# Performance work log

Measured on AMD Instinct MI355X. Metric: run time of the kernel, lower is better.

Reference implementation:

```python
import jax, jax.numpy as jnp
import numpy as np

B, S, D, F = 4, 4096, 512, 2048
EPS = 1e-5


def _layer_norm(x, g, b):
    # LayerNorm((sqlength, mdim)): normalize jointly over last two dims
    mu = jnp.mean(x, axis=(-2, -1), keepdims=True)
    var = jnp.mean(jnp.square(x - mu), axis=(-2, -1), keepdims=True)
    return (x - mu) * jax.lax.rsqrt(var + EPS) * g + b


def _attn(q, k, v, causal):
    # scores: [B, S_q, S_k]
    s = jnp.einsum('bqd,bkd->bqk', q, k) / jnp.sqrt(jnp.asarray(D, q.dtype))
    if causal:
        mask = jnp.triu(jnp.ones((s.shape[-2], s.shape[-1]), dtype=bool), k=1)
        s = jnp.where(mask, -jnp.inf, s)
    p = jax.nn.softmax(s, axis=-1)
    return jnp.einsum('bqk,bkd->bqd', p, v)


def setup_inputs() -> dict:
    key = jax.random.key(0)
    ks = jax.random.split(key, 12)
    sc = 0.02
    return {
        'x':    jax.random.normal(ks[0], (B, S, D), jnp.float32),
        'enc':  jax.random.normal(ks[1], (B, S, D), jnp.float32),
        'Wo1':  jax.random.normal(ks[2], (D, D), jnp.float32) * sc,
        'Wo2':  jax.random.normal(ks[3], (D, D), jnp.float32) * sc,
        'ln1_g': jnp.ones((S, D), jnp.float32),
        'ln1_b': jnp.zeros((S, D), jnp.float32),
        'ln2_g': jnp.ones((S, D), jnp.float32),
        'ln2_b': jnp.zeros((S, D), jnp.float32),
        'W1':   jax.random.normal(ks[4], (F, D), jnp.float32) * sc,
        'b1':   jnp.zeros((F,), jnp.float32),
        'W2':   jax.random.normal(ks[5], (D, F), jnp.float32) * sc,
        'b2':   jnp.zeros((D,), jnp.float32),
    }


def reference(x, enc, Wo1, Wo2, ln1_g, ln1_b, ln2_g, ln2_b, W1, b1, W2, b2):
    # 1) causal self-attention + residual + ln1
    o = _attn(x, x, x, causal=True) @ Wo1.T
    x = _layer_norm(o + x, ln1_g, ln1_b)
    # 2) cross attention (q=enc, k=enc, v=x per source) + residual + ln2
    o = _attn(enc, enc, x, causal=False) @ Wo2.T
    x = _layer_norm(o + x, ln2_g, ln2_b)
    # 3) position-wise FFN (original looped per token; vectorized here) + residual + ln2 (shared params)
    ff = jax.nn.relu(x @ W1.T + b1) @ W2.T + b2
    return _layer_norm(ff + x, ln2_g, ln2_b)
```

## Files before the change

### kernel.cpp

```cpp
#include <hip/hip_runtime.h>
#include <cstdint>
#include <cstddef>

#define NB 4
#define NS 4096
#define ND 512
#define NF 2048

typedef __bf16 bf16;
typedef __attribute__((ext_vector_type(8))) __bf16 bf16x8;
typedef __attribute__((ext_vector_type(4))) __bf16 bf16x4;
typedef __attribute__((ext_vector_type(4))) float f32x4;

#define MFMA16(a, b, c) __builtin_amdgcn_mfma_f32_16x16x32_bf16((a), (b), (c), 0, 0, 0)

__device__ __forceinline__ void async_copy16(void* lds, const void* g) {
  __builtin_amdgcn_global_load_lds(
      (__attribute__((address_space(1))) unsigned int*)(uintptr_t)g,
      (__attribute__((address_space(3))) unsigned int*)(unsigned)(uintptr_t)lds,
      16, 0, 0);
}

__device__ __forceinline__ int vswz_col(int c , int dloc) {
  return (c & ~31) | (((((c >> 3) & 3) + ((dloc >> 1) & 3)) & 3) << 3);
}

__global__ void k_detect(const unsigned short* __restrict__ x, unsigned* __restrict__ flag) {
  __shared__ int cnt;
  if (threadIdx.x == 0) cnt = 0;
  __syncthreads();
  int bad = 0;
  for (int i = threadIdx.x; i < 2048; i += 256) {
    unsigned e = (x[i] >> 7) & 0xFF;
    if (e < 100 || e > 140) bad++;
  }
  atomicAdd(&cnt, bad);
  __syncthreads();
  if (threadIdx.x == 0) *flag = (cnt > 200) ? 1u : 0u;
}

__global__ void k_norm_bf16(const void* __restrict__ src, bf16* __restrict__ dst,
                            const unsigned* __restrict__ flag, int n) {
  int i = (blockIdx.x * 256 + threadIdx.x) * 8;
  if (i >= n) return;
  if (*flag) {
    const float* s = (const float*)src;
    float4 a = *(const float4*)(s + i);
    float4 c = *(const float4*)(s + i + 4);
    bf16x8 v;
    v[0] = (bf16)a.x; v[1] = (bf16)a.y; v[2] = (bf16)a.z; v[3] = (bf16)a.w;
    v[4] = (bf16)c.x; v[5] = (bf16)c.y; v[6] = (bf16)c.z; v[7] = (bf16)c.w;
    *(bf16x8*)(dst + i) = v;
  } else {
    *(uint4*)(dst + i) = *(const uint4*)((const bf16*)src + i);
  }
}

__global__ void k_norm_f32(const void* __restrict__ src, float* __restrict__ dst,
                           const unsigned* __restrict__ flag, int n) {
  int i = blockIdx.x * 256 + threadIdx.x;
  if (i >= n) return;
  dst[i] = (*flag) ? ((const float*)src)[i] : (float)((const bf16*)src)[i];
}

__global__ void k_transpose(const bf16* __restrict__ in, bf16* __restrict__ out) {
  __shared__ bf16 t[64][72];
  const int b = blockIdx.z, s0 = blockIdx.x * 64, d0 = blockIdx.y * 64;
  const int tid = threadIdx.x;
#pragma unroll
  for (int it = 0; it < 2; ++it) {
    int slot = it * 256 + tid;
    int r = slot >> 3, c = (slot & 7) * 8;
    *(bf16x8*)&t[r][c] = *(const bf16x8*)&in[((size_t)b * NS + s0 + r) * ND + d0 + c];
  }
  __syncthreads();
#pragma unroll
  for (int it = 0; it < 2; ++it) {
    int slot = it * 256 + tid;
    int r = slot >> 3, c = (slot & 7) * 8;
    bf16x8 v;
#pragma unroll
    for (int k = 0; k < 8; ++k) v[k] = t[c + k][r];
    *(bf16x8*)&out[((size_t)b * ND + d0 + r) * NS + s0 + vswz_col(c, r)] = v;
  }
}

template <bool CAUSAL>
__global__ __launch_bounds__(512, 2) void k_attn7(const bf16* __restrict__ Q,
                                                  const bf16* __restrict__ Km,
                                                  const bf16* __restrict__ Vt,
                                                  bf16* __restrict__ O0, bf16* __restrict__ O1,
                                                  float2* __restrict__ ml) {
  __shared__ bf16 lds_[65536];

  const int tid = threadIdx.x;
  const int w = tid >> 6, lane = tid & 63, quad = lane >> 4, l15 = lane & 15;
  const int slot = blockIdx.x & 7;
  const int b = slot >> 1;
  const int z = slot & 1;
  const int q0 = (int)(blockIdx.x >> 3) * 128;

  const bf16* Kg = Km + (size_t)b * NS * ND;
  const bf16* Vg = Vt + (size_t)b * ND * NS;

  const bf16* Qg = Q + ((size_t)b * NS + q0 + w * 16 + l15) * ND;
  bf16x8 qf[16];
#pragma unroll
  for (int s = 0; s < 16; ++s) qf[s] = *(const bf16x8*)&Qg[s * 32 + quad * 8];
#pragma unroll
  for (int s = 0; s < 16; ++s)
#pragma unroll
    for (int j = 0; j < 8; ++j) qf[s][j] = (bf16)((float)qf[s][j] * 0.044194173824159216f);

  f32x4 o[32];
#pragma unroll
  for (int i = 0; i < 32; ++i) o[i] = (f32x4){0.f, 0.f, 0.f, 0.f};

  float m = -1e30f, l = 0.f;

  const int T = CAUSAL ? (q0 / 32 + 4) : (NS / 32);
  const int tA = (T + 1) >> 1;
  const int kt0 = z ? tA : 0;
  const int kt1 = z ? T : tA;
  const int laneA4 = ((((quad * 2) & 3) * 16) + l15) * 4;
  const int laneB4 = ((((quad * 2 + 1) & 3) * 16) + l15) * 4;
  const int vsw = ((quad + ((l15 >> 1) & 3)) & 3) * 8;

  auto STAGE = [&](bf16* base, int k0) {
#pragma unroll
    for (int i = 0; i < 4; ++i) {
      const int r = w * 4 + i;
      const int g = (lane & ~7) | ((lane ^ r) & 7);
      async_copy16(base + r * 512, Kg + (size_t)(k0 + r) * ND + g * 8);
    }
#pragma unroll
    for (int i = 0; i < 4; ++i) {
      const int d0 = (w * 4 + i) * 16;
      async_copy16(base + 16384 + d0 * 32, Vg + (size_t)(d0 + (lane >> 2)) * NS + k0 + (lane & 3) * 8);
    }
  };

  int buf = 0;
  if (kt0 < kt1) STAGE(lds_, kt0 * 32);
  __syncthreads();

  for (int kt = kt0; kt < kt1; ++kt) {
    const int k0 = kt * 32;
    bf16* Ks = lds_ + buf * 32768;
    bf16* Vs = Ks + 16384;
    if (kt + 1 < kt1) STAGE(lds_ + (buf ^ 1) * 32768, (kt + 1) * 32);

    f32x4 sa0 = (f32x4){0.f, 0.f, 0.f, 0.f};
    f32x4 sa1 = (f32x4){0.f, 0.f, 0.f, 0.f};
    __builtin_amdgcn_s_setprio(1);
#pragma unroll
    for (int s = 0; s < 16; ++s) {
      const int lc = s * 4 + quad;
      const int swz = ((lc & ~7) | ((lc ^ l15) & 7)) * 8;
      bf16x8 a0 = *(const bf16x8*)&Ks[l15 * 512 + swz];
      bf16x8 a1 = *(const bf16x8*)&Ks[(16 + l15) * 512 + swz];
      sa0 = MFMA16(a0, qf[s], sa0);
      sa1 = MFMA16(a1, qf[s], sa1);
    }
    __builtin_amdgcn_s_setprio(0);

    float sv[8];
    {
      const int qrow = q0 + w * 16 + l15;
      const bool needMask = CAUSAL && (k0 + 31 > q0 + w * 16);
#pragma unroll
      for (int kt2 = 0; kt2 < 2; ++kt2)
#pragma unroll
        for (int r = 0; r < 4; ++r) {
          float s = (kt2 == 0) ? sa0[r] : sa1[r];
          if (needMask) {
            int key = k0 + kt2 * 16 + quad * 4 + r;
            if (key > qrow) s = -1e30f;
          }
          sv[kt2 * 4 + r] = s;
        }
    }
    float tm = sv[0];
#pragma unroll
    for (int i = 1; i < 8; ++i) tm = fmaxf(tm, sv[i]);
    tm = fmaxf(tm, __shfl_xor(tm, 16));
    tm = fmaxf(tm, __shfl_xor(tm, 32));
    const float mn = fmaxf(m, tm);
    const float alpha = __expf(m - mn);
    m = mn;
    float pf[8];
    float ts = 0.f;
#pragma unroll
    for (int i = 0; i < 8; ++i) { pf[i] = __expf(sv[i] - mn); ts += pf[i]; }
    ts += __shfl_xor(ts, 16);
    ts += __shfl_xor(ts, 32);
    l = l * alpha + ts;
    if (__ballot(alpha < 0.99999f)) {
#pragma unroll
      for (int dt = 0; dt < 32; ++dt)
#pragma unroll
        for (int r = 0; r < 4; ++r) o[dt][r] *= alpha;
    }

    bf16x8 pb;
#pragma unroll
    for (int j = 0; j < 8; ++j) {
      const int r_ = j & 3;
      const int sl = (j < 4) ? laneA4 : laneB4;
      float v0 = __int_as_float(__builtin_amdgcn_ds_bpermute(sl, __float_as_int(pf[r_])));
      float v1 = __int_as_float(__builtin_amdgcn_ds_bpermute(sl, __float_as_int(pf[4 + r_])));
      pb[j] = (bf16)(quad < 2 ? v0 : v1);
    }

    __builtin_amdgcn_s_setprio(1);
#pragma unroll
    for (int dt = 0; dt < 32; ++dt) {
      bf16x8 a = *(const bf16x8*)&Vs[(dt * 16 + l15) * 32 + vsw];
      o[dt] = MFMA16(a, pb, o[dt]);
    }
    __builtin_amdgcn_s_setprio(0);

    __syncthreads();
    buf ^= 1;
  }

  const float inv = 1.f / l;
  if (lane < 16 && quad == 0) ml[((size_t)z * NB + b) * NS + q0 + w * 16 + lane] = make_float2(m, l);
  bf16* Ow = lds_ + w * 8192;
#pragma unroll
  for (int dt = 0; dt < 32; ++dt) {
    bf16x4 v;
#pragma unroll
    for (int r = 0; r < 4; ++r) v[r] = (bf16)(o[dt][r] * inv);
    *(bf16x4*)&Ow[l15 * 512 + dt * 16 + quad * 4] = v;
  }
  bf16* Og = (z ? O1 : O0) + ((size_t)b * NS + q0 + w * 16) * ND;
#pragma unroll
  for (int it = 0; it < 16; ++it) {
    bf16x8 row = *(const bf16x8*)&Ow[it * 512 + lane * 8];
    *(bf16x8*)&Og[(size_t)it * ND + lane * 8] = row;
  }
}

__global__ void k_merge(bf16* __restrict__ O0, const bf16* __restrict__ O1,
                        const float2* __restrict__ ml) {
  size_t i = ((size_t)blockIdx.x * 256 + threadIdx.x) * 8;
  int row = (int)(i >> 9);
  float2 a = ml[row];
  float2 c = ml[(size_t)NB * NS + row];
  float M = fmaxf(a.x, c.x);
  float w0 = __expf(a.x - M) * a.y;
  float w1 = __expf(c.x - M) * c.y;
  float den = 1.f / (w0 + w1);
  float c0 = w0 * den, c1 = w1 * den;
  bf16x8 v0 = *(const bf16x8*)(O0 + i);
  bf16x8 v1 = *(const bf16x8*)(O1 + i);
  bf16x8 ov;
#pragma unroll
  for (int k = 0; k < 8; ++k) ov[k] = (bf16)(c0 * (float)v0[k] + c1 * (float)v1[k]);
  *(bf16x8*)(O0 + i) = ov;
}

template <int RES_MODE, bool HAS_BIAS, bool RELU, bool STATS>
__global__ __launch_bounds__(256) void k_gemm(const bf16* __restrict__ A, const bf16* __restrict__ W,
                                              const bf16* __restrict__ resid,
                                              const float* __restrict__ bias, bf16* __restrict__ Out,
                                              float* __restrict__ stats, int M, int N, int K,
                                              int rowOfs) {
  __shared__ bf16 As[128 * 64];
  __shared__ bf16 Ws[128 * 64];
  const int tid = threadIdx.x;
  const int w = tid >> 6, lane = tid & 63, quad = lane >> 4, l15 = lane & 15;
  const int m0 = blockIdx.x * 128, n0 = blockIdx.y * 128;
  const int wr = (w >> 1) * 64, wc = (w & 1) * 64;
  const int arow = lane >> 3, acol = (lane & 7) * 8;

  f32x4 acc[16];
#pragma unroll
  for (int i = 0; i < 16; ++i) acc[i] = (f32x4){0.f, 0.f, 0.f, 0.f};

  for (int k0 = 0; k0 < K; k0 += 64) {
    __syncthreads();
#pragma unroll
    for (int i = 0; i < 4; ++i) {
      const int rbase = (w * 4 + i) * 8 + arow;
      async_copy16(&As[(w * 4 + i) * 512], A + (size_t)(m0 + rbase) * K + k0 + acol);
      async_copy16(&Ws[(w * 4 + i) * 512], W + (size_t)(n0 + rbase) * K + k0 + acol);
    }
    __syncthreads();
#pragma unroll
    for (int s = 0; s < 2; ++s) {
      bf16x8 af[4], bw[4];
#pragma unroll
      for (int i = 0; i < 4; ++i) af[i] = *(const bf16x8*)&As[(wr + i * 16 + l15) * 64 + s * 32 + quad * 8];
#pragma unroll
      for (int j = 0; j < 4; ++j) bw[j] = *(const bf16x8*)&Ws[(wc + j * 16 + l15) * 64 + s * 32 + quad * 8];
#pragma unroll
      for (int i = 0; i < 4; ++i)
#pragma unroll
        for (int j = 0; j < 4; ++j) acc[i * 4 + j] = MFMA16(af[i], bw[j], acc[i * 4 + j]);
    }
  }

  float lsum = 0.f, lsq = 0.f;
#pragma unroll
  for (int i = 0; i < 4; ++i)
#pragma unroll
    for (int j = 0; j < 4; ++j)
#pragma unroll
      for (int r = 0; r < 4; ++r) {
        int row = m0 + wr + i * 16 + quad * 4 + r;
        int col = n0 + wc + j * 16 + l15;
        float v = acc[i * 4 + j][r];
        if (HAS_BIAS) v += bias[col];
        if (RELU) v = fmaxf(v, 0.f);
        if (RES_MODE == 2) v += (float)resid[(size_t)row * N + col];
        Out[(size_t)row * N + col] = (bf16)v;
        if (STATS) { lsum += v; lsq += v * v; }
      }

  if (STATS) {
    __syncthreads();
    float* red = (float*)As;
    red[tid] = lsum;
    red[256 + tid] = lsq;
    __syncthreads();
    for (int off = 128; off > 0; off >>= 1) {
      if (tid < off) { red[tid] += red[tid + off]; red[256 + tid] += red[256 + tid + off]; }
      __syncthreads();
    }
    if (tid == 0) {
      int bidx = (rowOfs + m0) >> 12;
      atomicAdd(&stats[bidx * 2], red[0]);
      atomicAdd(&stats[bidx * 2 + 1], red[256]);
    }
  }
}

template <bool FINAL>
__global__ void k_ln(const bf16* __restrict__ T, const float* __restrict__ stats,
                     const void* __restrict__ gp, const void* __restrict__ bp,
                     void* __restrict__ outp, const unsigned* __restrict__ flag) {
  const float invN = 1.f / 2097152.f;
  size_t i = ((size_t)(blockIdx.x * 256 + threadIdx.x)) * 8;
  int b = (int)(i >> 21);
  int sd = (int)(i & 2097151);
  float mu = stats[b * 2] * invN;
  float var = stats[b * 2 + 1] * invN - mu * mu;
  float rs = rsqrtf(var + 1e-5f);
  bool f32m = (*flag != 0);
  bf16x8 tv = *(const bf16x8*)(T + i);
  float gv[8], bv[8];
  if (f32m) {
    float4 a = *(const float4*)((const float*)gp + sd), c = *(const float4*)((const float*)gp + sd + 4);
    gv[0] = a.x; gv[1] = a.y; gv[2] = a.z; gv[3] = a.w; gv[4] = c.x; gv[5] = c.y; gv[6] = c.z; gv[7] = c.w;
    float4 e = *(const float4*)((const float*)bp + sd), f = *(const float4*)((const float*)bp + sd + 4);
    bv[0] = e.x; bv[1] = e.y; bv[2] = e.z; bv[3] = e.w; bv[4] = f.x; bv[5] = f.y; bv[6] = f.z; bv[7] = f.w;
  } else {
    bf16x8 g8 = *(const bf16x8*)((const bf16*)gp + sd);
    bf16x8 b8 = *(const bf16x8*)((const bf16*)bp + sd);
#pragma unroll
    for (int k = 0; k < 8; ++k) { gv[k] = (float)g8[k]; bv[k] = (float)b8[k]; }
  }
  float ov[8];
#pragma unroll
  for (int k = 0; k < 8; ++k) ov[k] = ((float)tv[k] - mu) * rs * gv[k] + bv[k];
  if (FINAL && f32m) {
    float4 o0 = {ov[0], ov[1], ov[2], ov[3]}, o1 = {ov[4], ov[5], ov[6], ov[7]};
    *(float4*)((float*)outp + i) = o0;
    *(float4*)((float*)outp + i + 4) = o1;
  } else {
    bf16x8 o8;
#pragma unroll
    for (int k = 0; k < 8; ++k) o8[k] = (bf16)ov[k];
    *(bf16x8*)((bf16*)outp + i) = o8;
  }
}

__global__ void k_ln_t(const bf16* __restrict__ T, const float* __restrict__ stats,
                       const void* __restrict__ gp, const void* __restrict__ bp,
                       bf16* __restrict__ X, bf16* __restrict__ XT,
                       const unsigned* __restrict__ flag) {
  __shared__ bf16 t[64][72];
  const float invN = 1.f / 2097152.f;
  const int b = blockIdx.z, s0 = blockIdx.x * 64, d0 = blockIdx.y * 64;
  const int tid = threadIdx.x;
  const float mu = stats[b * 2] * invN;
  const float var = stats[b * 2 + 1] * invN - mu * mu;
  const float rs = rsqrtf(var + 1e-5f);
  const bool f32m = (*flag != 0);
#pragma unroll
  for (int it = 0; it < 2; ++it) {
    int slot = it * 256 + tid;
    int r = slot >> 3, c = (slot & 7) * 8;
    size_t idx = ((size_t)b * NS + s0 + r) * ND + d0 + c;
    size_t pidx = (size_t)(s0 + r) * ND + d0 + c;
    bf16x8 tv = *(const bf16x8*)&T[idx];
    float gv[8], bv[8];
    if (f32m) {
      float4 a = *(const float4*)((const float*)gp + pidx), cc = *(const float4*)((const float*)gp + pidx + 4);
      gv[0] = a.x; gv[1] = a.y; gv[2] = a.z; gv[3] = a.w; gv[4] = cc.x; gv[5] = cc.y; gv[6] = cc.z; gv[7] = cc.w;
      float4 e = *(const float4*)((const float*)bp + pidx), f = *(const float4*)((const float*)bp + pidx + 4);
      bv[0] = e.x; bv[1] = e.y; bv[2] = e.z; bv[3] = e.w; bv[4] = f.x; bv[5] = f.y; bv[6] = f.z; bv[7] = f.w;
    } else {
      bf16x8 g8 = *(const bf16x8*)((const bf16*)gp + pidx);
      bf16x8 b8 = *(const bf16x8*)((const bf16*)bp + pidx);
#pragma unroll
      for (int k = 0; k < 8; ++k) { gv[k] = (float)g8[k]; bv[k] = (float)b8[k]; }
    }
    bf16x8 ov;
#pragma unroll
    for (int k = 0; k < 8; ++k) ov[k] = (bf16)(((float)tv[k] - mu) * rs * gv[k] + bv[k]);
    *(bf16x8*)&X[idx] = ov;
    *(bf16x8*)&t[r][c] = ov;
  }
  __syncthreads();
#pragma unroll
  for (int it = 0; it < 2; ++it) {
    int slot = it * 256 + tid;
    int r = slot >> 3, c = (slot & 7) * 8;
    bf16x8 v;
#pragma unroll
    for (int k = 0; k < 8; ++k) v[k] = t[c + k][r];
    *(bf16x8*)&XT[((size_t)b * ND + d0 + r) * NS + s0 + vswz_col(c, r)] = v;
  }
}

extern "C" void kernel_launch(void* const* d_in, const int* in_sizes, int n_in, void* d_out,
                              int out_size, void* d_ws, size_t ws_size, hipStream_t stream) {
  (void)in_sizes; (void)n_in; (void)out_size;
  const void* x_raw = d_in[0];
  const void* enc_raw = d_in[1];
  const void* Wo1_raw = d_in[2];
  const void* Wo2_raw = d_in[3];
  const void* g1_raw = d_in[4];
  const void* bb1_raw = d_in[5];
  const void* g2_raw = d_in[6];
  const void* bb2_raw = d_in[7];
  const void* W1_raw = d_in[8];
  const void* bias1_raw = d_in[9];
  const void* W2_raw = d_in[10];
  const void* bias2_raw = d_in[11];

  char* w = (char*)d_ws;
  unsigned* flag = (unsigned*)(w + 0);
  float* stats = (float*)(w + 16);
  float* b1f = (float*)(w + 1024);
  float* b2f = (float*)(w + 1024 + 8192);
  size_t off = 16384;
  const size_t nBSD = (size_t)NB * NS * ND;
  bf16* Wo1b = (bf16*)(w + off); off += (size_t)ND * ND * 2;
  bf16* Wo2b = (bf16*)(w + off); off += (size_t)ND * ND * 2;
  bf16* W1b = (bf16*)(w + off); off += (size_t)NF * ND * 2;
  bf16* W2b = (bf16*)(w + off); off += (size_t)ND * NF * 2;
  bf16* xb = (bf16*)(w + off); off += nBSD * 2;
  bf16* Ab = (bf16*)(w + off); off += nBSD * 2;
  bf16* Tb = (bf16*)(w + off); off += nBSD * 2;
  bf16* X1b = (bf16*)(w + off); off += nBSD * 2;
  bf16* Hb = (bf16*)(w + off);
  const size_t hbFull = (size_t)NB * NS * NF * 2;
  const size_t hbHalf = hbFull / 2;
  const bool ffnFull = (ws_size >= off + hbFull);
  if (!ffnFull && ws_size < off + hbHalf) return;

  bf16* O1b = Hb;
  float2* mlb = (float2*)((char*)Hb + nBSD * 2);

  hipMemsetAsync(stats, 0, 24 * sizeof(float), stream);
  k_detect<<<1, 256, 0, stream>>>((const unsigned short*)x_raw, flag);

  k_norm_bf16<<<(int)(nBSD / 2048), 256, 0, stream>>>(x_raw, xb, flag, (int)nBSD);
  k_norm_bf16<<<(ND * ND) / 2048, 256, 0, stream>>>(Wo1_raw, Wo1b, flag, ND * ND);
  k_norm_bf16<<<(ND * ND) / 2048, 256, 0, stream>>>(Wo2_raw, Wo2b, flag, ND * ND);
  k_norm_bf16<<<(NF * ND) / 2048, 256, 0, stream>>>(W1_raw, W1b, flag, NF * ND);
  k_norm_bf16<<<(NF * ND) / 2048, 256, 0, stream>>>(W2_raw, W2b, flag, ND * NF);
  k_norm_f32<<<8, 256, 0, stream>>>(bias1_raw, b1f, flag, NF);
  k_norm_f32<<<2, 256, 0, stream>>>(bias2_raw, b2f, flag, ND);

  k_transpose<<<dim3(NS / 64, ND / 64, NB), 256, 0, stream>>>(xb, Tb);
  k_attn7<true><<<256, 512, 0, stream>>>(xb, xb, Tb, Ab, O1b, mlb);
  k_merge<<<(int)(nBSD / 2048), 256, 0, stream>>>(Ab, O1b, mlb);
  k_gemm<2, false, false, true><<<dim3(128, 4), 256, 0, stream>>>(Ab, Wo1b, xb, nullptr, Tb,
                                                                  stats + 0, NB * NS, ND, ND, 0);
  k_ln_t<<<dim3(NS / 64, ND / 64, NB), 256, 0, stream>>>(Tb, stats + 0, g1_raw, bb1_raw, X1b, Ab,
                                                         flag);
  k_norm_bf16<<<(int)(nBSD / 2048), 256, 0, stream>>>(enc_raw, xb, flag, (int)nBSD);

  k_attn7<false><<<256, 512, 0, stream>>>(xb, xb, Ab, Tb, O1b, mlb);
  k_merge<<<(int)(nBSD / 2048), 256, 0, stream>>>(Tb, O1b, mlb);
  k_gemm<2, false, false, true><<<dim3(128, 4), 256, 0, stream>>>(Tb, Wo2b, X1b, nullptr, Ab,
                                                                  stats + 8, NB * NS, ND, ND, 0);
  k_ln<false><<<(int)(nBSD / 2048), 256, 0, stream>>>(Ab, stats + 8, g2_raw, bb2_raw, X1b, flag);

  const int nChunk = ffnFull ? 1 : 2;
  const int rows = ffnFull ? (NB * NS) : 8192;
  for (int c = 0; c < nChunk; ++c) {
    size_t ro = (size_t)c * rows;
    k_gemm<0, true, true, false><<<dim3(rows / 128, 16), 256, 0, stream>>>(
        X1b + ro * ND, W1b, nullptr, b1f, Hb, nullptr, rows, NF, ND, 0);
    k_gemm<2, true, false, true><<<dim3(rows / 128, 4), 256, 0, stream>>>(
        Hb, W2b, X1b + ro * ND, b2f, Tb + ro * ND, stats + 16, rows, ND, NF, (int)ro);
  }
  k_ln<true><<<(int)(nBSD / 2048), 256, 0, stream>>>(Tb, stats + 16, g2_raw, bb2_raw, d_out, flag);
}
```

Baseline: 795.9 us.

## Balance causal attention by pairing low and high query tiles per block

Each causal attention block now covers two 64-row query groups taken from opposite ends of the sequence (j and 63-j). Warps 0-3 handle the low group and warps 4-7 the high one, and the two groups' key tiles run back to back in a single loop. Every block therefore processes a fixed 65 key tiles instead of a count that grows with query position, which removes the tail imbalance of the causal triangle. The cost is that half the warps sit idle at barriers in each iteration while the other half compute, so per-CU MFMA utilisation may drop.

```diff
diff --git a/kernel.cpp b/kernel.cpp
--- a/kernel.cpp
+++ b/kernel.cpp
@@ -86,7 +86,7 @@
 }
 
 template <bool CAUSAL>
-__global__ __launch_bounds__(512, 2) void k_attn7(const bf16* __restrict__ Q,
+__global__ __launch_bounds__(512, 2) void k_attn8(const bf16* __restrict__ Q,
                                                   const bf16* __restrict__ Km,
                                                   const bf16* __restrict__ Vt,
                                                   bf16* __restrict__ O0, bf16* __restrict__ O1,
@@ -98,19 +98,36 @@
   const int slot = blockIdx.x & 7;
   const int b = slot >> 1;
   const int z = slot & 1;
-  const int q0 = (int)(blockIdx.x >> 3) * 128;
+  const int j = (int)(blockIdx.x >> 3);
+
+  int qwb, nLo, n;
+  if (CAUSAL) {
+    nLo = j + 1;
+    n = 65;
+    qwb = (w < 4) ? (64 * j + w * 16) : (4032 - 64 * j + (w - 4) * 16);
+  } else {
+    nLo = 1 << 30;
+    n = 64;
+    qwb = j * 128 + w * 16;
+  }
+  const int nHi = 64 - j;
 
   const bf16* Kg = Km + (size_t)b * NS * ND;
   const bf16* Vg = Vt + (size_t)b * ND * NS;
 
-  const bf16* Qg = Q + ((size_t)b * NS + q0 + w * 16 + l15) * ND;
+  auto ktOf = [&](int i) -> int {
+    if (!CAUSAL) return z * 64 + i;
+    return (i < nLo) ? (z * nLo + i) : (z * nHi + (i - nLo));
+  };
+
+  const bf16* Qg = Q + ((size_t)b * NS + qwb + l15) * ND;
   bf16x8 qf[16];
 #pragma unroll
   for (int s = 0; s < 16; ++s) qf[s] = *(const bf16x8*)&Qg[s * 32 + quad * 8];
 #pragma unroll
   for (int s = 0; s < 16; ++s)
 #pragma unroll
-    for (int j = 0; j < 8; ++j) qf[s][j] = (bf16)((float)qf[s][j] * 0.044194173824159216f);
+    for (int jj = 0; jj < 8; ++jj) qf[s][jj] = (bf16)((float)qf[s][jj] * 0.044194173824159216f);
 
   f32x4 o[32];
 #pragma unroll
@@ -118,10 +135,6 @@
 
   float m = -1e30f, l = 0.f;
 
-  const int T = CAUSAL ? (q0 / 32 + 4) : (NS / 32);
-  const int tA = (T + 1) >> 1;
-  const int kt0 = z ? tA : 0;
-  const int kt1 = z ? T : tA;
   const int laneA4 = ((((quad * 2) & 3) * 16) + l15) * 4;
   const int laneB4 = ((((quad * 2 + 1) & 3) * 16) + l15) * 4;
   const int vsw = ((quad + ((l15 >> 1) & 3)) & 3) * 8;
@@ -141,91 +154,94 @@
   };
 
   int buf = 0;
-  if (kt0 < kt1) STAGE(lds_, kt0 * 32);
+  STAGE(lds_, ktOf(0) * 32);
   __syncthreads();
 
-  for (int kt = kt0; kt < kt1; ++kt) {
-    const int k0 = kt * 32;
+  for (int i = 0; i < n; ++i) {
+    const int k0 = ktOf(i) * 32;
     bf16* Ks = lds_ + buf * 32768;
     bf16* Vs = Ks + 16384;
-    if (kt + 1 < kt1) STAGE(lds_ + (buf ^ 1) * 32768, (kt + 1) * 32);
-
-    f32x4 sa0 = (f32x4){0.f, 0.f, 0.f, 0.f};
-    f32x4 sa1 = (f32x4){0.f, 0.f, 0.f, 0.f};
-    __builtin_amdgcn_s_setprio(1);
-#pragma unroll
-    for (int s = 0; s < 16; ++s) {
-      const int lc = s * 4 + quad;
-      const int swz = ((lc & ~7) | ((lc ^ l15) & 7)) * 8;
-      bf16x8 a0 = *(const bf16x8*)&Ks[l15 * 512 + swz];
-      bf16x8 a1 = *(const bf16x8*)&Ks[(16 + l15) * 512 + swz];
-      sa0 = MFMA16(a0, qf[s], sa0);
-      sa1 = MFMA16(a1, qf[s], sa1);
-    }
-    __builtin_amdgcn_s_setprio(0);
-
-    float sv[8];
-    {
-      const int qrow = q0 + w * 16 + l15;
-      const bool needMask = CAUSAL && (k0 + 31 > q0 + w * 16);
-#pragma unroll
-      for (int kt2 = 0; kt2 < 2; ++kt2)
-#pragma unroll
-        for (int r = 0; r < 4; ++r) {
-          float s = (kt2 == 0) ? sa0[r] : sa1[r];
-          if (needMask) {
-            int key = k0 + kt2 * 16 + quad * 4 + r;
-            if (key > qrow) s = -1e30f;
+    if (i + 1 < n) STAGE(lds_ + (buf ^ 1) * 32768, ktOf(i + 1) * 32);
+
+    const bool active = !CAUSAL || ((w >= 4) == (i >= nLo));
+    if (active) {
+      f32x4 sa0 = (f32x4){0.f, 0.f, 0.f, 0.f};
+      f32x4 sa1 = (f32x4){0.f, 0.f, 0.f, 0.f};
+      __builtin_amdgcn_s_setprio(1);
+#pragma unroll
+      for (int s = 0; s < 16; ++s) {
+        const int lc = s * 4 + quad;
+        const int swz = ((lc & ~7) | ((lc ^ l15) & 7)) * 8;
+        bf16x8 a0 = *(const bf16x8*)&Ks[l15 * 512 + swz];
+        bf16x8 a1 = *(const bf16x8*)&Ks[(16 + l15) * 512 + swz];
+        sa0 = MFMA16(a0, qf[s], sa0);
+        sa1 = MFMA16(a1, qf[s], sa1);
+      }
+      __builtin_amdgcn_s_setprio(0);
+
+      float sv[8];
+      {
+        const int qrow = qwb + l15;
+        const bool needMask = CAUSAL && (k0 + 31 > qwb);
+#pragma unroll
+        for (int kt2 = 0; kt2 < 2; ++kt2)
+#pragma unroll
+          for (int r = 0; r < 4; ++r) {
+            float s = (kt2 == 0) ? sa0[r] : sa1[r];
+            if (needMask) {
+              int key = k0 + kt2 * 16 + quad * 4 + r;
+              if (key > qrow) s = -1e30f;
+            }
+            sv[kt2 * 4 + r] = s;
           }
-          sv[kt2 * 4 + r] = s;
-        }
-    }
-    float tm = sv[0];
-#pragma unroll
-    for (int i = 1; i < 8; ++i) tm = fmaxf(tm, sv[i]);
-    tm = fmaxf(tm, __shfl_xor(tm, 16));
-    tm = fmaxf(tm, __shfl_xor(tm, 32));
-    const float mn = fmaxf(m, tm);
-    const float alpha = __expf(m - mn);
-    m = mn;
-    float pf[8];
-    float ts = 0.f;
-#pragma unroll
-    for (int i = 0; i < 8; ++i) { pf[i] = __expf(sv[i] - mn); ts += pf[i]; }
-    ts += __shfl_xor(ts, 16);
-    ts += __shfl_xor(ts, 32);
-    l = l * alpha + ts;
-    if (__ballot(alpha < 0.99999f)) {
-#pragma unroll
-      for (int dt = 0; dt < 32; ++dt)
-#pragma unroll
-        for (int r = 0; r < 4; ++r) o[dt][r] *= alpha;
-    }
-
-    bf16x8 pb;
-#pragma unroll
-    for (int j = 0; j < 8; ++j) {
-      const int r_ = j & 3;
-      const int sl = (j < 4) ? laneA4 : laneB4;
-      float v0 = __int_as_float(__builtin_amdgcn_ds_bpermute(sl, __float_as_int(pf[r_])));
-      float v1 = __int_as_float(__builtin_amdgcn_ds_bpermute(sl, __float_as_int(pf[4 + r_])));
-      pb[j] = (bf16)(quad < 2 ? v0 : v1);
-    }
-
-    __builtin_amdgcn_s_setprio(1);
-#pragma unroll
-    for (int dt = 0; dt < 32; ++dt) {
-      bf16x8 a = *(const bf16x8*)&Vs[(dt * 16 + l15) * 32 + vsw];
-      o[dt] = MFMA16(a, pb, o[dt]);
-    }
-    __builtin_amdgcn_s_setprio(0);
+      }
+      float tm = sv[0];
+#pragma unroll
+      for (int i2 = 1; i2 < 8; ++i2) tm = fmaxf(tm, sv[i2]);
+      tm = fmaxf(tm, __shfl_xor(tm, 16));
+      tm = fmaxf(tm, __shfl_xor(tm, 32));
+      const float mn = fmaxf(m, tm);
+      const float alpha = __expf(m - mn);
+      m = mn;
+      float pf[8];
+      float ts = 0.f;
+#pragma unroll
+      for (int i2 = 0; i2 < 8; ++i2) { pf[i2] = __expf(sv[i2] - mn); ts += pf[i2]; }
+      ts += __shfl_xor(ts, 16);
+      ts += __shfl_xor(ts, 32);
+      l = l * alpha + ts;
+      if (__ballot(alpha < 0.99999f)) {
+#pragma unroll
+        for (int dt = 0; dt < 32; ++dt)
+#pragma unroll
+          for (int r = 0; r < 4; ++r) o[dt][r] *= alpha;
+      }
+
+      bf16x8 pb;
+#pragma unroll
+      for (int jj = 0; jj < 8; ++jj) {
+        const int r_ = jj & 3;
+        const int sl = (jj < 4) ? laneA4 : laneB4;
+        float v0 = __int_as_float(__builtin_amdgcn_ds_bpermute(sl, __float_as_int(pf[r_])));
+        float v1 = __int_as_float(__builtin_amdgcn_ds_bpermute(sl, __float_as_int(pf[4 + r_])));
+        pb[jj] = (bf16)(quad < 2 ? v0 : v1);
+      }
+
+      __builtin_amdgcn_s_setprio(1);
+#pragma unroll
+      for (int dt = 0; dt < 32; ++dt) {
+        bf16x8 a = *(const bf16x8*)&Vs[(dt * 16 + l15) * 32 + vsw];
+        o[dt] = MFMA16(a, pb, o[dt]);
+      }
+      __builtin_amdgcn_s_setprio(0);
+    }
 
     __syncthreads();
     buf ^= 1;
   }
 
   const float inv = 1.f / l;
-  if (lane < 16 && quad == 0) ml[((size_t)z * NB + b) * NS + q0 + w * 16 + lane] = make_float2(m, l);
+  if (lane < 16 && quad == 0) ml[((size_t)z * NB + b) * NS + qwb + lane] = make_float2(m, l);
   bf16* Ow = lds_ + w * 8192;
 #pragma unroll
   for (int dt = 0; dt < 32; ++dt) {
@@ -234,7 +250,7 @@
     for (int r = 0; r < 4; ++r) v[r] = (bf16)(o[dt][r] * inv);
     *(bf16x4*)&Ow[l15 * 512 + dt * 16 + quad * 4] = v;
   }
-  bf16* Og = (z ? O1 : O0) + ((size_t)b * NS + q0 + w * 16) * ND;
+  bf16* Og = (z ? O1 : O0) + ((size_t)b * NS + qwb) * ND;
 #pragma unroll
   for (int it = 0; it < 16; ++it) {
     bf16x8 row = *(const bf16x8*)&Ow[it * 512 + lane * 8];
@@ -294,11 +310,11 @@
 #pragma unroll
       for (int i = 0; i < 4; ++i) af[i] = *(const bf16x8*)&As[(wr + i * 16 + l15) * 64 + s * 32 + quad * 8];
 #pragma unroll
-      for (int j = 0; j < 4; ++j) bw[j] = *(const bf16x8*)&Ws[(wc + j * 16 + l15) * 64 + s * 32 + quad * 8];
+      for (int jj = 0; jj < 4; ++jj) bw[jj] = *(const bf16x8*)&Ws[(wc + jj * 16 + l15) * 64 + s * 32 + quad * 8];
 #pragma unroll
       for (int i = 0; i < 4; ++i)
 #pragma unroll
-        for (int j = 0; j < 4; ++j) acc[i * 4 + j] = MFMA16(af[i], bw[j], acc[i * 4 + j]);
+        for (int jj = 0; jj < 4; ++jj) acc[i * 4 + jj] = MFMA16(af[i], bw[jj], acc[i * 4 + jj]);
     }
   }
 
@@ -306,12 +322,12 @@
 #pragma unroll
   for (int i = 0; i < 4; ++i)
 #pragma unroll
-    for (int j = 0; j < 4; ++j)
+    for (int jj = 0; jj < 4; ++jj)
 #pragma unroll
       for (int r = 0; r < 4; ++r) {
         int row = m0 + wr + i * 16 + quad * 4 + r;
-        int col = n0 + wc + j * 16 + l15;
-        float v = acc[i * 4 + j][r];
+        int col = n0 + wc + jj * 16 + l15;
+        float v = acc[i * 4 + jj][r];
         if (HAS_BIAS) v += bias[col];
         if (RELU) v = fmaxf(v, 0.f);
         if (RES_MODE == 2) v += (float)resid[(size_t)row * N + col];
@@ -478,7 +494,7 @@
   k_norm_f32<<<2, 256, 0, stream>>>(bias2_raw, b2f, flag, ND);
 
   k_transpose<<<dim3(NS / 64, ND / 64, NB), 256, 0, stream>>>(xb, Tb);
-  k_attn7<true><<<256, 512, 0, stream>>>(xb, xb, Tb, Ab, O1b, mlb);
+  k_attn8<true><<<256, 512, 0, stream>>>(xb, xb, Tb, Ab, O1b, mlb);
   k_merge<<<(int)(nBSD / 2048), 256, 0, stream>>>(Ab, O1b, mlb);
   k_gemm<2, false, false, true><<<dim3(128, 4), 256, 0, stream>>>(Ab, Wo1b, xb, nullptr, Tb,
                                                                   stats + 0, NB * NS, ND, ND, 0);
@@ -486,7 +502,7 @@
                                                          flag);
   k_norm_bf16<<<(int)(nBSD / 2048), 256, 0, stream>>>(enc_raw, xb, flag, (int)nBSD);
 
-  k_attn7<false><<<256, 512, 0, stream>>>(xb, xb, Ab, Tb, O1b, mlb);
+  k_attn8<false><<<256, 512, 0, stream>>>(xb, xb, Ab, Tb, O1b, mlb);
   k_merge<<<(int)(nBSD / 2048), 256, 0, stream>>>(Tb, O1b, mlb);
   k_gemm<2, false, false, true><<<dim3(128, 4), 256, 0, stream>>>(Tb, Wo2b, X1b, nullptr, Ab,
                                                                   stats + 8, NB * NS, ND, ND, 0);
```

Measured after the change: 783.7 us. About the same (-1.5%).
